# Optimization experiments

Hardware: AMD Instinct MI355X
Metric: run time of the kernel (lower is better)

## Reference

```python
import jax, jax.numpy as jnp
import numpy as np

L = 2
H = 2          # attn heads
E = 4          # embed dim
D = E // H     # head dim
FFN = 16
V = 8
B, S = 32, 1024
EPS = 1e-5


def setup_inputs() -> dict:
    key = jax.random.key(0)
    ks = jax.random.split(key, 8)
    return {
        "token_ids": jax.random.randint(ks[0], (B, S), 0, V),
        "emb": jax.random.normal(ks[1], (V, E), jnp.float32),
        "ln1_g": jnp.ones((L, E), jnp.float32),
        "ln1_b": jnp.zeros((L, E), jnp.float32),
        "wqkv": jax.random.normal(ks[2], (L, 3 * E, E), jnp.float32) * 0.5,
        "wo": jax.random.normal(ks[3], (L, E, E), jnp.float32) * 0.5,
        "ln2_g": jnp.ones((L, E), jnp.float32),
        "ln2_b": jnp.zeros((L, E), jnp.float32),
        "w1": jax.random.normal(ks[4], (L, FFN, E), jnp.float32) * 0.5,
        "b1": jnp.zeros((L, FFN), jnp.float32),
        "w2": jax.random.normal(ks[5], (L, E, FFN), jnp.float32) * 0.5,
        "b2": jnp.zeros((L, E), jnp.float32),
        "out_w": jax.random.normal(ks[6], (V, E), jnp.float32),
    }


def _layernorm(x, g, b):
    mu = jnp.mean(x, axis=-1, keepdims=True)
    var = jnp.mean(jnp.square(x - mu), axis=-1, keepdims=True)
    return (x - mu) * jax.lax.rsqrt(var + EPS) * g + b


def _block(x, g1, b1n, wqkv, wo, g2, b2n, w1, b1, w2, b2):
    # --- self-attention sublayer ---
    h = _layernorm(x, g1, b1n)                       # [B,S,E]
    qkv = jnp.einsum("bse,fe->bsf", h, wqkv)        # [B,S,3E]
    q, k, v = jnp.split(qkv, 3, axis=-1)
    q = q.reshape(B, S, H, D)
    k = k.reshape(B, S, H, D)
    v = v.reshape(B, S, H, D)
    scores = jnp.einsum("bqhd,bkhd->bhqk", q, k) / jnp.sqrt(jnp.float32(D))
    attn = jax.nn.softmax(scores, axis=-1)           # [B,H,S,S]
    o = jnp.einsum("bhqk,bkhd->bqhd", attn, v).reshape(B, S, E)
    x = x + jnp.einsum("bse,fe->bsf", o, wo)
    # --- FFN sublayer ---
    h = _layernorm(x, g2, b2n)
    h = jax.nn.gelu(jnp.einsum("bse,fe->bsf", h, w1) + b1, approximate=False)
    return x + jnp.einsum("bsf,ef->bse", h, w2) + b2


def reference(token_ids, emb, ln1_g, ln1_b, wqkv, wo, ln2_g, ln2_b, w1, b1, w2, b2, out_w):
    x = emb[token_ids]                               # [B,S,E]
    for l in range(L):
        x = _block(x, ln1_g[l], ln1_b[l], wqkv[l], wo[l],
                   ln2_g[l], ln2_b[l], w1[l], b1[l], w2[l], b2[l])
    return jnp.einsum("bse,ve->bsv", x, out_w)       # [B,S,V]
```

## Files before the change

kernel.cpp:

```cpp
#include <hip/hip_runtime.h>
#include <math.h>


#define Bz  32
#define Sz  1024
#define Lz  2
#define Ez  4
#define Hz  2
#define Dz  2
#define FFNz 16
#define Vz  8
#define EPSz 1e-5f

#define CHUNKS 8
#define POSPC (Sz / CHUNKS)
#define NT 256

__device__ __forceinline__ void layernorm4(const float* x, const float* g,
                                           const float* b, float* h) {
    float mu = 0.25f * (x[0] + x[1] + x[2] + x[3]);
    float d0 = x[0] - mu, d1 = x[1] - mu, d2 = x[2] - mu, d3 = x[3] - mu;
    float var = 0.25f * (d0 * d0 + d1 * d1 + d2 * d2 + d3 * d3);
    float r = 1.0f / sqrtf(var + EPSz);
    h[0] = d0 * r * g[0] + b[0];
    h[1] = d1 * r * g[1] + b[1];
    h[2] = d2 * r * g[2] + b[2];
    h[3] = d3 * r * g[3] + b[3];
}

__global__ __launch_bounds__(NT) void tformer_collapse(
    const int* __restrict__ tok,
    const float* __restrict__ emb,
    const float* __restrict__ ln1_g, const float* __restrict__ ln1_b,
    const float* __restrict__ wqkv, const float* __restrict__ wo,
    const float* __restrict__ ln2_g, const float* __restrict__ ln2_b,
    const float* __restrict__ w1, const float* __restrict__ b1,
    const float* __restrict__ w2, const float* __restrict__ b2,
    const float* __restrict__ out_w,
    float* __restrict__ out)
{
    __shared__ int   toks[Sz];
    __shared__ int   hist[Vz];
    __shared__ float kv_k[Vz][Ez];
    __shared__ float kv_v[Vz][Ez];
    __shared__ __align__(16) float table[Vz][Vz];

    const int b     = blockIdx.x / CHUNKS;
    const int chunk = blockIdx.x % CHUNKS;
    const int tid   = threadIdx.x;

    if (tid < Vz) hist[tid] = 0;
    __syncthreads();

    const int* tb = tok + b * Sz;
    #pragma unroll
    for (int k = 0; k < Sz / NT; ++k) {
        int t = tb[tid + k * NT];
        toks[tid + k * NT] = t;
        atomicAdd(&hist[t], 1);
    }
    __syncthreads();

    float x[Ez];
    float cnt[Vz];
    const int t = tid;
    if (tid < Vz) {
        #pragma unroll
        for (int e = 0; e < Ez; ++e) x[e] = emb[t * Ez + e];
        #pragma unroll
        for (int j = 0; j < Vz; ++j) cnt[j] = (float)hist[j];
    }

    #pragma unroll
    for (int l = 0; l < Lz; ++l) {
        float q[Ez];
        if (tid < Vz) {
            float h[Ez];
            layernorm4(x, ln1_g + l * Ez, ln1_b + l * Ez, h);
            const float* wq = wqkv + l * 3 * Ez * Ez;
            #pragma unroll
            for (int f = 0; f < Ez; ++f) {
                float sq = 0.f, sk = 0.f, sv = 0.f;
                #pragma unroll
                for (int e = 0; e < Ez; ++e) {
                    sq += wq[f * Ez + e] * h[e];
                    sk += wq[(Ez + f) * Ez + e] * h[e];
                    sv += wq[(2 * Ez + f) * Ez + e] * h[e];
                }
                q[f] = sq;
                kv_k[t][f] = sk;
                kv_v[t][f] = sv;
            }
        }
        __syncthreads();

        if (tid < Vz) {
            float o[Ez];
            #pragma unroll
            for (int hh = 0; hh < Hz; ++hh) {
                float sc[Vz];
                float m = -1e30f;
                #pragma unroll
                for (int j = 0; j < Vz; ++j) {
                    float s = 0.f;
                    #pragma unroll
                    for (int d = 0; d < Dz; ++d)
                        s += q[hh * Dz + d] * kv_k[j][hh * Dz + d];
                    s *= 0.70710678118654752f;
                    sc[j] = s;
                    m = fmaxf(m, s);
                }
                float Z = 0.f;
                float acc0 = 0.f, acc1 = 0.f;
                #pragma unroll
                for (int j = 0; j < Vz; ++j) {
                    float w = cnt[j] * expf(sc[j] - m);
                    Z += w;
                    acc0 += w * kv_v[j][hh * Dz + 0];
                    acc1 += w * kv_v[j][hh * Dz + 1];
                }
                o[hh * Dz + 0] = acc0 / Z;
                o[hh * Dz + 1] = acc1 / Z;
            }
            #pragma unroll
            for (int f = 0; f < Ez; ++f) {
                float s = 0.f;
                #pragma unroll
                for (int e = 0; e < Ez; ++e)
                    s += o[e] * wo[(l * Ez + f) * Ez + e];
                x[f] += s;
            }
            float h2[Ez];
            layernorm4(x, ln2_g + l * Ez, ln2_b + l * Ez, h2);
            float a0 = 0.f, a1 = 0.f, a2 = 0.f, a3 = 0.f;
            #pragma unroll
            for (int f = 0; f < FFNz; ++f) {
                float u = b1[l * FFNz + f];
                #pragma unroll
                for (int e = 0; e < Ez; ++e)
                    u += w1[(l * FFNz + f) * Ez + e] * h2[e];
                float g = 0.5f * u * (1.0f + erff(u * 0.70710678118654752f));
                a0 += g * w2[(l * Ez + 0) * FFNz + f];
                a1 += g * w2[(l * Ez + 1) * FFNz + f];
                a2 += g * w2[(l * Ez + 2) * FFNz + f];
                a3 += g * w2[(l * Ez + 3) * FFNz + f];
            }
            x[0] += a0 + b2[l * Ez + 0];
            x[1] += a1 + b2[l * Ez + 1];
            x[2] += a2 + b2[l * Ez + 2];
            x[3] += a3 + b2[l * Ez + 3];
        }
        __syncthreads();
    }

    if (tid < Vz) {
        #pragma unroll
        for (int vv = 0; vv < Vz; ++vv) {
            float s = 0.f;
            #pragma unroll
            for (int e = 0; e < Ez; ++e) s += x[e] * out_w[vv * Ez + e];
            table[t][vv] = s;
        }
    }
    __syncthreads();

    const int posBase = chunk * POSPC;
    const int p    = tid >> 1;
    const int part = tid & 1;
    const int tk   = toks[posBase + p];
    float4 val = ((const float4*)&table[tk][0])[part];
    float4* out4 = (float4*)(out + ((size_t)b * Sz + posBase) * Vz);
    out4[tid] = val;
}

extern "C" void kernel_launch(void* const* d_in, const int* in_sizes, int n_in,
                              void* d_out, int out_size, void* d_ws, size_t ws_size,
                              hipStream_t stream) {
    const int*   tok   = (const int*)  d_in[0];
    const float* emb   = (const float*)d_in[1];
    const float* ln1_g = (const float*)d_in[2];
    const float* ln1_b = (const float*)d_in[3];
    const float* wqkv  = (const float*)d_in[4];
    const float* wo    = (const float*)d_in[5];
    const float* ln2_g = (const float*)d_in[6];
    const float* ln2_b = (const float*)d_in[7];
    const float* w1    = (const float*)d_in[8];
    const float* b1    = (const float*)d_in[9];
    const float* w2    = (const float*)d_in[10];
    const float* b2    = (const float*)d_in[11];
    const float* out_w = (const float*)d_in[12];
    float* out = (float*)d_out;

    dim3 grid(Bz * CHUNKS);
    dim3 block(NT);
    tformer_collapse<<<grid, block, 0, stream>>>(
        tok, emb, ln1_g, ln1_b, wqkv, wo, ln2_g, ln2_b,
        w1, b1, w2, b2, out_w, out);
}
```

Baseline: 89.40 us.

## Stage weights in LDS, use ballot histogram, parallelize per-token layers across threads

Weights are preloaded into shared memory cooperatively, and the token loads are issued early so they overlap with the weight loads. The per-token histogram now uses wave ballot/popcount instead of per-element shared atomics. The serial per-vocab computation is split across more threads: attention per (token, head), FFN per (token, hidden unit) with a shuffle reduction, and the output table per (token, vocab). This shortens the serial critical path at the cost of extra barriers and shared-memory traffic.

Result: faster. 82.84 us (-7.3%).

```diff
diff --git a/kernel.cpp b/kernel.cpp
--- a/kernel.cpp
+++ b/kernel.cpp
@@ -41,8 +41,22 @@
 {
     __shared__ int   toks[Sz];
     __shared__ int   hist[Vz];
+    __shared__ float s_wqkv[Lz * 3 * Ez * Ez];
+    __shared__ float s_w1[Lz * FFNz * Ez];
+    __shared__ float s_emb[Vz * Ez];
+    __shared__ float s_w2[Lz * Ez * FFNz];
+    __shared__ float s_wo[Lz * Ez * Ez];
+    __shared__ float s_outw[Vz * Ez];
+    __shared__ float s_b1[Lz * FFNz];
+    __shared__ float s_b2[Lz * Ez];
+    __shared__ float s_ln1g[Lz * Ez], s_ln1b[Lz * Ez];
+    __shared__ float s_ln2g[Lz * Ez], s_ln2b[Lz * Ez];
+    __shared__ float sx[Vz][Ez];
+    __shared__ float sq[Vz][Ez];
     __shared__ float kv_k[Vz][Ez];
     __shared__ float kv_v[Vz][Ez];
+    __shared__ float so[Vz][Ez];
+    __shared__ float sh2[Vz][Ez];
     __shared__ __align__(16) float table[Vz][Vz];
 
     const int b     = blockIdx.x / CHUNKS;
@@ -50,117 +64,156 @@
     const int tid   = threadIdx.x;
 
     if (tid < Vz) hist[tid] = 0;
+
+    const int* tb = tok + b * Sz;
+    int tkr[Sz / NT];
+    #pragma unroll
+    for (int k = 0; k < Sz / NT; ++k) tkr[k] = tb[tid + k * NT];
+
+    if (tid < 96)        s_wqkv[tid]      = wqkv[tid];
+    else if (tid < 224)  s_w1[tid - 96]   = w1[tid - 96];
+    else                 s_emb[tid - 224] = emb[tid - 224];
+
+    if (tid < 128)       s_w2[tid]          = w2[tid];
+    else if (tid < 160)  s_wo[tid - 128]    = wo[tid - 128];
+    else if (tid < 192)  s_outw[tid - 160]  = out_w[tid - 160];
+    else if (tid < 224)  s_b1[tid - 192]    = b1[tid - 192];
+    else if (tid < 232)  s_b2[tid - 224]    = b2[tid - 224];
+    else if (tid < 240)  s_ln1g[tid - 232]  = ln1_g[tid - 232];
+    else if (tid < 248)  s_ln1b[tid - 240]  = ln1_b[tid - 240];
+    else                 s_ln2g[tid - 248]  = ln2_g[tid - 248];
+    if (tid < 8)         s_ln2b[tid]        = ln2_b[tid];
+
     __syncthreads();
 
-    const int* tb = tok + b * Sz;
+    int c[Vz] = {0, 0, 0, 0, 0, 0, 0, 0};
     #pragma unroll
     for (int k = 0; k < Sz / NT; ++k) {
-        int t = tb[tid + k * NT];
+        int t = tkr[k];
         toks[tid + k * NT] = t;
-        atomicAdd(&hist[t], 1);
+        #pragma unroll
+        for (int v = 0; v < Vz; ++v)
+            c[v] += (int)__popcll(__ballot(t == v));
+    }
+    if ((tid & 63) == 0) {
+        #pragma unroll
+        for (int v = 0; v < Vz; ++v) atomicAdd(&hist[v], c[v]);
     }
     __syncthreads();
 
-    float x[Ez];
-    float cnt[Vz];
-    const int t = tid;
+    float cntr[Vz];
+    if (tid < Vz * Hz) {
+        #pragma unroll
+        for (int j = 0; j < Vz; ++j) cntr[j] = (float)hist[j];
+    }
     if (tid < Vz) {
         #pragma unroll
-        for (int e = 0; e < Ez; ++e) x[e] = emb[t * Ez + e];
-        #pragma unroll
-        for (int j = 0; j < Vz; ++j) cnt[j] = (float)hist[j];
+        for (int e = 0; e < Ez; ++e) sx[tid][e] = s_emb[tid * Ez + e];
     }
 
     #pragma unroll
     for (int l = 0; l < Lz; ++l) {
-        float q[Ez];
         if (tid < Vz) {
+            const int t = tid;
             float h[Ez];
-            layernorm4(x, ln1_g + l * Ez, ln1_b + l * Ez, h);
-            const float* wq = wqkv + l * 3 * Ez * Ez;
+            layernorm4(&sx[t][0], s_ln1g + l * Ez, s_ln1b + l * Ez, h);
+            const float* wq = s_wqkv + l * 3 * Ez * Ez;
             #pragma unroll
             for (int f = 0; f < Ez; ++f) {
-                float sq = 0.f, sk = 0.f, sv = 0.f;
+                float aq = 0.f, ak = 0.f, av = 0.f;
                 #pragma unroll
                 for (int e = 0; e < Ez; ++e) {
-                    sq += wq[f * Ez + e] * h[e];
-                    sk += wq[(Ez + f) * Ez + e] * h[e];
-                    sv += wq[(2 * Ez + f) * Ez + e] * h[e];
+                    aq += wq[f * Ez + e] * h[e];
+                    ak += wq[(Ez + f) * Ez + e] * h[e];
+                    av += wq[(2 * Ez + f) * Ez + e] * h[e];
                 }
-                q[f] = sq;
-                kv_k[t][f] = sk;
-                kv_v[t][f] = sv;
-            }
+                sq[t][f]   = aq;
+                kv_k[t][f] = ak;
+                kv_v[t][f] = av;
+            }
+        }
+        __syncthreads();
+
+        if (tid < Vz * Hz) {
+            const int t = tid >> 1, hh = tid & 1;
+            const float q0 = sq[t][hh * Dz + 0], q1 = sq[t][hh * Dz + 1];
+            float sc[Vz];
+            float m = -1e30f;
+            #pragma unroll
+            for (int j = 0; j < Vz; ++j) {
+                float s = (q0 * kv_k[j][hh * Dz + 0] +
+                           q1 * kv_k[j][hh * Dz + 1]) * 0.70710678118654752f;
+                sc[j] = s;
+                m = fmaxf(m, s);
+            }
+            float Z = 0.f, a0 = 0.f, a1 = 0.f;
+            #pragma unroll
+            for (int j = 0; j < Vz; ++j) {
+                float w = cntr[j] * expf(sc[j] - m);
+                Z  += w;
+                a0 += w * kv_v[j][hh * Dz + 0];
+                a1 += w * kv_v[j][hh * Dz + 1];
+            }
+            so[t][hh * Dz + 0] = a0 / Z;
+            so[t][hh * Dz + 1] = a1 / Z;
         }
         __syncthreads();
 
         if (tid < Vz) {
-            float o[Ez];
-            #pragma unroll
-            for (int hh = 0; hh < Hz; ++hh) {
-                float sc[Vz];
-                float m = -1e30f;
-                #pragma unroll
-                for (int j = 0; j < Vz; ++j) {
-                    float s = 0.f;
-                    #pragma unroll
-                    for (int d = 0; d < Dz; ++d)
-                        s += q[hh * Dz + d] * kv_k[j][hh * Dz + d];
-                    s *= 0.70710678118654752f;
-                    sc[j] = s;
-                    m = fmaxf(m, s);
-                }
-                float Z = 0.f;
-                float acc0 = 0.f, acc1 = 0.f;
-                #pragma unroll
-                for (int j = 0; j < Vz; ++j) {
-                    float w = cnt[j] * expf(sc[j] - m);
-                    Z += w;
-                    acc0 += w * kv_v[j][hh * Dz + 0];
-                    acc1 += w * kv_v[j][hh * Dz + 1];
-                }
-                o[hh * Dz + 0] = acc0 / Z;
-                o[hh * Dz + 1] = acc1 / Z;
-            }
+            const int t = tid;
+            float x[Ez], o[Ez];
+            #pragma unroll
+            for (int e = 0; e < Ez; ++e) { x[e] = sx[t][e]; o[e] = so[t][e]; }
             #pragma unroll
             for (int f = 0; f < Ez; ++f) {
                 float s = 0.f;
                 #pragma unroll
                 for (int e = 0; e < Ez; ++e)
-                    s += o[e] * wo[(l * Ez + f) * Ez + e];
+                    s += o[e] * s_wo[(l * Ez + f) * Ez + e];
                 x[f] += s;
             }
+            #pragma unroll
+            for (int e = 0; e < Ez; ++e) sx[t][e] = x[e];
             float h2[Ez];
-            layernorm4(x, ln2_g + l * Ez, ln2_b + l * Ez, h2);
-            float a0 = 0.f, a1 = 0.f, a2 = 0.f, a3 = 0.f;
-            #pragma unroll
-            for (int f = 0; f < FFNz; ++f) {
-                float u = b1[l * FFNz + f];
-                #pragma unroll
-                for (int e = 0; e < Ez; ++e)
-                    u += w1[(l * FFNz + f) * Ez + e] * h2[e];
-                float g = 0.5f * u * (1.0f + erff(u * 0.70710678118654752f));
-                a0 += g * w2[(l * Ez + 0) * FFNz + f];
-                a1 += g * w2[(l * Ez + 1) * FFNz + f];
-                a2 += g * w2[(l * Ez + 2) * FFNz + f];
-                a3 += g * w2[(l * Ez + 3) * FFNz + f];
-            }
-            x[0] += a0 + b2[l * Ez + 0];
-            x[1] += a1 + b2[l * Ez + 1];
-            x[2] += a2 + b2[l * Ez + 2];
-            x[3] += a3 + b2[l * Ez + 3];
-        }
-        __syncthreads();
-    }
-
-    if (tid < Vz) {
-        #pragma unroll
-        for (int vv = 0; vv < Vz; ++vv) {
-            float s = 0.f;
-            #pragma unroll
-            for (int e = 0; e < Ez; ++e) s += x[e] * out_w[vv * Ez + e];
-            table[t][vv] = s;
-        }
+            layernorm4(x, s_ln2g + l * Ez, s_ln2b + l * Ez, h2);
+            #pragma unroll
+            for (int e = 0; e < Ez; ++e) sh2[t][e] = h2[e];
+        }
+        __syncthreads();
+
+        if (tid < Vz * FFNz) {
+            const int t = tid >> 4, f = tid & 15;
+            const float* w1r = s_w1 + (l * FFNz + f) * Ez;
+            float u = s_b1[l * FFNz + f]
+                    + w1r[0] * sh2[t][0] + w1r[1] * sh2[t][1]
+                    + w1r[2] * sh2[t][2] + w1r[3] * sh2[t][3];
+            float g = 0.5f * u * (1.0f + erff(u * 0.70710678118654752f));
+            float r0 = g * s_w2[(l * Ez + 0) * FFNz + f];
+            float r1 = g * s_w2[(l * Ez + 1) * FFNz + f];
+            float r2 = g * s_w2[(l * Ez + 2) * FFNz + f];
+            float r3 = g * s_w2[(l * Ez + 3) * FFNz + f];
+            #pragma unroll
+            for (int msk = 1; msk < FFNz; msk <<= 1) {
+                r0 += __shfl_xor(r0, msk);
+                r1 += __shfl_xor(r1, msk);
+                r2 += __shfl_xor(r2, msk);
+                r3 += __shfl_xor(r3, msk);
+            }
+            if (f == 0) {
+                sx[t][0] += r0 + s_b2[l * Ez + 0];
+                sx[t][1] += r1 + s_b2[l * Ez + 1];
+                sx[t][2] += r2 + s_b2[l * Ez + 2];
+                sx[t][3] += r3 + s_b2[l * Ez + 3];
+            }
+        }
+        __syncthreads();
+    }
+
+    if (tid < Vz * Vz) {
+        const int t = tid >> 3, vv = tid & 7;
+        const float* ow = s_outw + vv * Ez;
+        table[t][vv] = sx[t][0] * ow[0] + sx[t][1] * ow[1]
+                     + sx[t][2] * ow[2] + sx[t][3] * ow[3];
     }
     __syncthreads();
 
```
